# Kernel tuning notes

Hardware: AMD Instinct MI355X
Metric: run time of the kernel (lower is better)

## Reference

```python
import jax, jax.numpy as jnp
import numpy as np

B, L, D = 8, 8192, 512
TARGET_RATIO = 1.0 / 6.0


def _normalize(v):
    # matches torch F.normalize(dim=-1, eps=1e-12)
    n = jnp.maximum(jnp.linalg.norm(v, axis=-1, keepdims=True), 1e-12)
    return v / n


def _downsample(x, b_hard):
    # vectorized stream compaction, padded to L (static upper bound of L_max)
    Bb, Ll, Dd = x.shape
    cnt = jnp.cumsum(b_hard.astype(jnp.int32), axis=1)
    pos = jnp.where(b_hard > 0.5, cnt - 1, Ll)          # non-selected -> dump slot L
    bidx = jnp.arange(Bb)[:, None]
    out = jnp.zeros((Bb, Ll + 1, Dd), x.dtype).at[bidx, pos].set(x)[:, :Ll]
    counts = cnt[:, -1]
    mask = jnp.arange(Ll)[None, :] < counts[:, None]
    return out, mask


def setup_inputs() -> dict:
    key = jax.random.key(0)
    k1, k2, k3 = jax.random.split(key, 3)
    x = jax.random.normal(k1, (B, L, D), jnp.float32)
    W_q = jax.random.normal(k2, (D, D), jnp.float32) / np.sqrt(D)
    W_k = jax.random.normal(k3, (D, D), jnp.float32) / np.sqrt(D)
    return {"x": x, "W_q": W_q, "W_k": W_k}


def reference(x, W_q, W_k):
    q = _normalize(jnp.einsum('bld,ed->ble', x, W_q))   # nn.Linear: x @ W.T
    k = _normalize(jnp.einsum('bld,ed->ble', x, W_k))
    k_prev = jnp.pad(k[:, :-1, :], ((0, 0), (1, 0), (0, 0)))
    cos_sim = jnp.sum(q * k_prev, axis=-1)               # (B, L)
    p = jnp.clip(0.5 * (1.0 - cos_sim), 0.0, 1.0)
    p = p.at[:, 0].set(1.0)                              # first position always boundary
    b_hard = (p >= 0.5).astype(x.dtype)
    N = 1.0 / TARGET_RATIO
    F_actual = jnp.mean(b_hard)
    G_actual = jnp.mean(p)
    ratio_loss = N / (N - 1.0) * ((N - 1.0) * F_actual * G_actual + (1.0 - F_actual) * (1.0 - G_actual))
    compressed, comp_mask = _downsample(x, b_hard)
    p_compressed, _ = _downsample(p[..., None], b_hard)
    p_compressed = p_compressed[..., 0]
    return (compressed, comp_mask, b_hard, p, p_compressed, ratio_loss)
```

## Files before the change

kernel.cpp:

```cpp
#include <hip/hip_runtime.h>
#include <hip/hip_bf16.h>
#include <math.h>

#define BB 8
#define LL 8192
#define DD 512
#define NROWS (BB * LL)

#define OUT_COMP   0
#define OUT_MASK   33554432
#define OUT_BHARD  33619968
#define OUT_P      33685504
#define OUT_PCOMP  33751040
#define OUT_LOSS   33816576

#define WS_FIXLIST 0
#define WS_FIXCNT  262144
#define WS_COUNTS  262148
#define WS_SUMP    262180
#define WS_SEL     262212
#define WS_SSK     524416
#define WS_SSQ     786560
#define WS_DOT     1048704
#define WS_WQH     1310848
#define WS_WQL     1835136
#define WS_WKH     2359424
#define WS_WKL     2883712

#define FIX_CAP 65536
#define FIX_TAU 1e-4f

typedef __attribute__((ext_vector_type(8))) _Float16 half8;
typedef __attribute__((ext_vector_type(4))) float f32x4;

static __device__ __forceinline__ void ld_g2l16(const void* g, void* l) {
  __builtin_amdgcn_global_load_lds(
      (const __attribute__((address_space(1))) void*)g,
      (__attribute__((address_space(3))) void*)l, 16, 0, 0);
}

__global__ __launch_bounds__(256) void wsplit(
    const float* __restrict__ Wq, const float* __restrict__ Wk,
    _Float16* __restrict__ wqh, _Float16* __restrict__ wql,
    _Float16* __restrict__ wkh, _Float16* __restrict__ wkl,
    float* __restrict__ ssk, float* __restrict__ ssq,
    float* __restrict__ dotb, int* __restrict__ fixcnt) {
  const int t = blockIdx.x * 256 + threadIdx.x;
  if (t == 0) *fixcnt = 0;
  ssk[t] = 0.0f;
  ssq[t] = 0.0f;
  dotb[t] = 0.0f;

  const int m = t >> 15;
  const int c = t & 32767;
  const int kt = c >> 11;
  const int ct = (c >> 6) & 31;
  const int l = c & 63;
  const int n = l & 15;
  const int kblk = l >> 4;
  const int e = ct * 16 + n;
  const int d0 = kt * 32 + kblk * 8;
  const float* src = (m ? Wk : Wq) + (long)e * 512 + d0;
  _Float16* dh = (m ? wkh : wqh) + (long)c * 8;
  _Float16* dl = (m ? wkl : wql) + (long)c * 8;
  float4 v0 = *(const float4*)src;
  float4 v1 = *(const float4*)(src + 4);
  float av[8] = {v0.x, v0.y, v0.z, v0.w, v1.x, v1.y, v1.z, v1.w};
  half8 hi, lo;
#pragma unroll
  for (int j = 0; j < 8; ++j) {
    _Float16 hh = (_Float16)av[j];
    hi[j] = hh;
    lo[j] = (_Float16)(av[j] - (float)hh);
  }
  *(half8*)dh = hi;
  *(half8*)dl = lo;
}

__global__ __launch_bounds__(256, 2) void gemm_fused(
    const float* __restrict__ x,
    const _Float16* __restrict__ wqh, const _Float16* __restrict__ wql,
    const _Float16* __restrict__ wkh, const _Float16* __restrict__ wkl,
    float* __restrict__ ssqOut, float* __restrict__ sskOut,
    float* __restrict__ dotOut,
    float* __restrict__ qedge, float* __restrict__ kedge) {
  __shared__ _Float16 smem[24576];
  _Float16* AH = smem;
  _Float16* AL = AH + 4096;
  _Float16* BQH = AL + 4096;
  _Float16* BQL = BQH + 4096;
  _Float16* BKH = BQL + 4096;
  _Float16* BKL = BKH + 4096;

  const int tid = threadIdx.x;
  const int lane = tid & 63;
  const int w = tid >> 6;
  const int wrow = w & 1, wcol = w >> 1;
  const int g = lane >> 4, n = lane & 15;
  const int bx = blockIdx.x;
  const int rb = bx >> 2, cb = bx & 3;
  const long r0 = (long)rb * 128;

  const int arow = ((tid >> 6) << 4) | (tid & 15);
  const int akb = (tid >> 4) & 3;
  const float* ap = x + (r0 + arow) * 512 + akb * 8;

  f32x4 accq[4][4], acck[4][4];
#pragma unroll
  for (int mb = 0; mb < 4; ++mb)
#pragma unroll
    for (int nb = 0; nb < 4; ++nb) {
      accq[mb][nb] = (f32x4){0.f, 0.f, 0.f, 0.f};
      acck[mb][nb] = (f32x4){0.f, 0.f, 0.f, 0.f};
    }

  float4 f0 = *(const float4*)(ap);
  float4 f1 = *(const float4*)(ap + 4);
  float4 f2 = *(const float4*)(ap + 64 * 512);
  float4 f3 = *(const float4*)(ap + 64 * 512 + 4);

  for (int kt = 0; kt < 16; ++kt) {
    const long bbase = ((long)(kt * 32 + cb * 8) << 9) + w * 1024 + lane * 8;
    ld_g2l16(wqh + bbase, BQH + w * 1024);
    ld_g2l16(wqh + bbase + 512, BQH + w * 1024 + 512);
    ld_g2l16(wql + bbase, BQL + w * 1024);
    ld_g2l16(wql + bbase + 512, BQL + w * 1024 + 512);
    ld_g2l16(wkh + bbase, BKH + w * 1024);
    ld_g2l16(wkh + bbase + 512, BKH + w * 1024 + 512);
    ld_g2l16(wkl + bbase, BKL + w * 1024);
    ld_g2l16(wkl + bbase + 512, BKL + w * 1024 + 512);
    {
      float av0[8] = {f0.x, f0.y, f0.z, f0.w, f1.x, f1.y, f1.z, f1.w};
      float av1[8] = {f2.x, f2.y, f2.z, f2.w, f3.x, f3.y, f3.z, f3.w};
      half8 h0, h1, l0, l1;
#pragma unroll
      for (int j = 0; j < 8; ++j) {
        _Float16 a = (_Float16)av0[j];
        h0[j] = a;
        l0[j] = (_Float16)(av0[j] - (float)a);
        _Float16 b = (_Float16)av1[j];
        h1[j] = b;
        l1[j] = (_Float16)(av1[j] - (float)b);
      }
      *(half8*)(AH + tid * 8) = h0;
      *(half8*)(AH + (tid + 256) * 8) = h1;
      *(half8*)(AL + tid * 8) = l0;
      *(half8*)(AL + (tid + 256) * 8) = l1;
    }
    __syncthreads();
    if (kt < 15) {
      const float* xp = ap + (kt + 1) * 32;
      f0 = *(const float4*)(xp);
      f1 = *(const float4*)(xp + 4);
      f2 = *(const float4*)(xp + 64 * 512);
      f3 = *(const float4*)(xp + 64 * 512 + 4);
    }
    half8 ah[4], al[4];
#pragma unroll
    for (int mb = 0; mb < 4; ++mb) {
      const int cm = wrow * 4 + mb;
      ah[mb] = *(const half8*)(AH + (cm * 64 + lane) * 8);
      al[mb] = *(const half8*)(AL + (cm * 64 + lane) * 8);
    }
    {
      half8 bh[4], bl[4];
#pragma unroll
      for (int nb = 0; nb < 4; ++nb) {
        bh[nb] = *(const half8*)(BQH + ((wcol * 4 + nb) * 64 + lane) * 8);
        bl[nb] = *(const half8*)(BQL + ((wcol * 4 + nb) * 64 + lane) * 8);
      }
#pragma unroll
      for (int nb = 0; nb < 4; ++nb)
#pragma unroll
        for (int mb = 0; mb < 4; ++mb) {
          accq[mb][nb] = __builtin_amdgcn_mfma_f32_16x16x32_f16(ah[mb], bh[nb], accq[mb][nb], 0, 0, 0);
          accq[mb][nb] = __builtin_amdgcn_mfma_f32_16x16x32_f16(al[mb], bh[nb], accq[mb][nb], 0, 0, 0);
          accq[mb][nb] = __builtin_amdgcn_mfma_f32_16x16x32_f16(ah[mb], bl[nb], accq[mb][nb], 0, 0, 0);
        }
    }
    {
      half8 bh[4], bl[4];
#pragma unroll
      for (int nb = 0; nb < 4; ++nb) {
        bh[nb] = *(const half8*)(BKH + ((wcol * 4 + nb) * 64 + lane) * 8);
        bl[nb] = *(const half8*)(BKL + ((wcol * 4 + nb) * 64 + lane) * 8);
      }
#pragma unroll
      for (int nb = 0; nb < 4; ++nb)
#pragma unroll
        for (int mb = 0; mb < 4; ++mb) {
          acck[mb][nb] = __builtin_amdgcn_mfma_f32_16x16x32_f16(ah[mb], bh[nb], acck[mb][nb], 0, 0, 0);
          acck[mb][nb] = __builtin_amdgcn_mfma_f32_16x16x32_f16(al[mb], bh[nb], acck[mb][nb], 0, 0, 0);
          acck[mb][nb] = __builtin_amdgcn_mfma_f32_16x16x32_f16(ah[mb], bl[nb], acck[mb][nb], 0, 0, 0);
        }
    }
    __syncthreads();
  }

  _Float16* KX = smem;
  const int col0 = wcol * 64 + n;
  const int rbase = wrow * 64;
#pragma unroll
  for (int mb = 0; mb < 4; ++mb)
#pragma unroll
    for (int reg = 0; reg < 4; ++reg) {
      const int rl = rbase + mb * 16 + g * 4 + reg;
#pragma unroll
      for (int nb = 0; nb < 4; ++nb)
        KX[rl * 136 + col0 + nb * 16] = (_Float16)acck[mb][nb][reg];
    }
  __syncthreads();

  if (wrow == 1 && g == 3) {
#pragma unroll
    for (int nb = 0; nb < 4; ++nb)
      kedge[rb * 512 + cb * 128 + col0 + nb * 16] = acck[3][nb][3];
  }
  if (wrow == 0 && g == 0) {
#pragma unroll
    for (int nb = 0; nb < 4; ++nb)
      qedge[rb * 512 + cb * 128 + col0 + nb * 16] = accq[0][nb][0];
  }

#pragma unroll
  for (int mb = 0; mb < 4; ++mb) {
#pragma unroll
    for (int reg = 0; reg < 4; ++reg) {
      const int rl = rbase + mb * 16 + g * 4 + reg;
      const long row = r0 + rl;
      float sq = 0.f, sk = 0.f, dt = 0.f;
#pragma unroll
      for (int nb = 0; nb < 4; ++nb) {
        float qv = accq[mb][nb][reg];
        float kv = acck[mb][nb][reg];
        sq = fmaf(qv, qv, sq);
        sk = fmaf(kv, kv, sk);
        if (rl > 0) {
          float kp = (float)KX[(rl - 1) * 136 + col0 + nb * 16];
          dt = fmaf(qv, kp, dt);
        }
      }
#pragma unroll
      for (int m = 1; m < 16; m <<= 1) {
        sq += __shfl_xor(sq, m, 64);
        sk += __shfl_xor(sk, m, 64);
        dt += __shfl_xor(dt, m, 64);
      }
      if (n == 0) {
        atomicAdd(&ssqOut[row], sq);
        atomicAdd(&sskOut[row], sk);
        if (rl > 0) atomicAdd(&dotOut[row], dt);
      }
    }
  }
}

__global__ __launch_bounds__(64) void edgedot(
    const float* __restrict__ qedge, const float* __restrict__ kedge,
    float* __restrict__ dotOut) {
  const int rb = blockIdx.x;
  if (rb == 0) return;
  const long row = (long)rb * 128;
  if ((row & (LL - 1)) == 0) return;
  const int lane = threadIdx.x;
  float dt = 0.f;
#pragma unroll
  for (int c = lane; c < 512; c += 64)
    dt = fmaf(qedge[rb * 512 + c], kedge[(rb - 1) * 512 + c], dt);
#pragma unroll
  for (int m = 1; m < 64; m <<= 1) dt += __shfl_xor(dt, m, 64);
  if (lane == 0) dotOut[row] = dt;
}

__global__ __launch_bounds__(256) void combine(
    const float* __restrict__ ssq, const float* __restrict__ ssk,
    const float* __restrict__ dotb, float* __restrict__ dout,
    int* __restrict__ fixlist, int* __restrict__ fixcnt) {
  const int r = blockIdx.x * 256 + threadIdx.x;
  const int l = r & (LL - 1);
  float p;
  float cosv = 0.0f;
  if (l != 0) {
    float nq = fmaxf(sqrtf(ssq[r]), 1e-12f);
    float nk = fmaxf(sqrtf(ssk[r - 1]), 1e-12f);
    cosv = dotb[r] / (nq * nk);
    p = fminf(fmaxf(0.5f * (1.0f - cosv), 0.0f), 1.0f);
  } else {
    p = 1.0f;
  }
  dout[OUT_P + r] = p;
  dout[OUT_BHARD + r] = (p >= 0.5f) ? 1.0f : 0.0f;
  if (l != 0 && fabsf(cosv) < FIX_TAU) {
    int idx = atomicAdd(fixcnt, 1);
    if (idx < FIX_CAP) fixlist[idx] = r;
  }
}

__global__ __launch_bounds__(256) void fixup(
    const float* __restrict__ x, const float* __restrict__ Wq,
    const float* __restrict__ Wk, float* __restrict__ dout,
    const int* __restrict__ fixlist, const int* __restrict__ fixcnt) {
  __shared__ float xr[512], xp[512];
  __shared__ double red[3][256];
  const int t = threadIdx.x;
  int nfix = *fixcnt;
  if (nfix > FIX_CAP) nfix = FIX_CAP;

  for (int idx = blockIdx.x; idx < nfix; idx += gridDim.x) {
    const int r = fixlist[idx];
    for (int d = t; d < 512; d += 256) {
      xr[d] = x[(long)r * 512 + d];
      xp[d] = x[(long)(r - 1) * 512 + d];
    }
    __syncthreads();
    double ssq = 0.0, ssk = 0.0, dot = 0.0;
    for (int e = t; e < 512; e += 256) {
      const float* wq = Wq + (long)e * 512;
      const float* wk = Wk + (long)e * 512;
      double q = 0.0, k = 0.0;
      for (int d = 0; d < 512; ++d) {
        q = fma((double)xr[d], (double)wq[d], q);
        k = fma((double)xp[d], (double)wk[d], k);
      }
      ssq += q * q;
      ssk += k * k;
      dot += q * k;
    }
    red[0][t] = ssq;
    red[1][t] = ssk;
    red[2][t] = dot;
    __syncthreads();
    for (int s = 128; s > 0; s >>= 1) {
      if (t < s) {
        red[0][t] += red[0][t + s];
        red[1][t] += red[1][t + s];
        red[2][t] += red[2][t + s];
      }
      __syncthreads();
    }
    if (t == 0) {
      double nq = sqrt(red[0][0]);
      double nk = sqrt(red[1][0]);
      if (nq < 1e-12) nq = 1e-12;
      if (nk < 1e-12) nk = 1e-12;
      float c = (float)(red[2][0] / (nq * nk));
      float p = fminf(fmaxf(0.5f * (1.0f - c), 0.0f), 1.0f);
      dout[OUT_P + r] = p;
      dout[OUT_BHARD + r] = (p >= 0.5f) ? 1.0f : 0.0f;
    }
    __syncthreads();
  }
}

__global__ __launch_bounds__(256) void scanb(
    float* __restrict__ dout, int* __restrict__ sel,
    int* __restrict__ counts, float* __restrict__ sump) {
  __shared__ int wtot[4];
  __shared__ float wps[4];
  const int b = blockIdx.x;
  const int t = threadIdx.x;
  const int lane = t & 63, wv = t >> 6;
  const long base = (long)b * LL;

  int cnt = 0;
  float psum = 0.0f;
#pragma unroll 4
  for (int j = 0; j < 32; ++j) {
    int l = t * 32 + j;
    float bh = dout[OUT_BHARD + base + l];
    float pv = dout[OUT_P + base + l];
    cnt += (bh > 0.5f) ? 1 : 0;
    psum += pv;
  }
  int inc = cnt;
#pragma unroll
  for (int off = 1; off < 64; off <<= 1) {
    int u = __shfl_up(inc, off, 64);
    if (lane >= off) inc += u;
  }
  float ps = psum;
#pragma unroll
  for (int off = 1; off < 64; off <<= 1) ps += __shfl_xor(ps, off, 64);
  if (lane == 63) wtot[wv] = inc;
  if (lane == 0) wps[wv] = ps;
  __syncthreads();
  int wbase = 0, total = 0;
#pragma unroll
  for (int i = 0; i < 4; ++i) {
    int c = wtot[i];
    if (i < wv) wbase += c;
    total += c;
  }
  if (t == 0) {
    counts[b] = total;
    sump[b] = wps[0] + wps[1] + wps[2] + wps[3];
  }
  for (int j = 0; j < 32; ++j) {
    int l = t * 32 + j;
    dout[OUT_MASK + base + l] = (l < total) ? 1.0f : 0.0f;
    dout[OUT_PCOMP + base + l] = 0.0f;
  }
  __syncthreads();
  int pos = wbase + inc - cnt;
  for (int j = 0; j < 32; ++j) {
    int l = t * 32 + j;
    float bh = dout[OUT_BHARD + base + l];
    if (bh > 0.5f) {
      dout[OUT_PCOMP + base + pos] = dout[OUT_P + base + l];
      sel[base + pos] = l;
      ++pos;
    }
  }
}

__global__ void lossk(float* __restrict__ dout, const int* __restrict__ counts,
                      const float* __restrict__ sump) {
  if (threadIdx.x == 0 && blockIdx.x == 0) {
    float fc = 0.0f, gs = 0.0f;
    for (int b = 0; b < BB; ++b) {
      fc += (float)counts[b];
      gs += sump[b];
    }
    float F = fc / (float)NROWS;
    float G = gs / (float)NROWS;
    dout[OUT_LOSS] = 1.2f * (5.0f * F * G + (1.0f - F) * (1.0f - G));
  }
}

__global__ __launch_bounds__(128) void emit(
    const float* __restrict__ x, float* __restrict__ dout,
    const int* __restrict__ sel, const int* __restrict__ counts) {
  const long bid = blockIdx.x;
  const int b = (int)(bid >> 13);
  const int j = (int)(bid & (LL - 1));
  const int cnt = counts[b];
  float4 v = make_float4(0.0f, 0.0f, 0.0f, 0.0f);
  if (j < cnt) {
    const int l = sel[((long)b << 13) + j];
    v = *(const float4*)(x + (((long)b << 13) + l) * 512 + threadIdx.x * 4);
  }
  *(float4*)(dout + OUT_COMP + (((long)b << 13) + j) * 512 + threadIdx.x * 4) = v;
}

extern "C" void kernel_launch(void* const* d_in, const int* in_sizes, int n_in,
                              void* d_out, int out_size, void* d_ws,
                              size_t ws_size, hipStream_t stream) {
  const float* x = (const float*)d_in[0];
  const float* Wq = (const float*)d_in[1];
  const float* Wk = (const float*)d_in[2];
  float* out = (float*)d_out;
  char* ws = (char*)d_ws;

  int* fixlist = (int*)(ws + WS_FIXLIST);
  int* fixcnt = (int*)(ws + WS_FIXCNT);
  int* counts = (int*)(ws + WS_COUNTS);
  float* sump = (float*)(ws + WS_SUMP);
  int* sel = (int*)(ws + WS_SEL);
  float* ssk = (float*)(ws + WS_SSK);
  float* ssq = (float*)(ws + WS_SSQ);
  float* dotb = (float*)(ws + WS_DOT);
  _Float16* wqh = (_Float16*)(ws + WS_WQH);
  _Float16* wql = (_Float16*)(ws + WS_WQL);
  _Float16* wkh = (_Float16*)(ws + WS_WKH);
  _Float16* wkl = (_Float16*)(ws + WS_WKL);

  float* kedge = (float*)(out + OUT_COMP);
  float* qedge = (float*)(out + OUT_COMP + 262144);

  wsplit<<<256, 256, 0, stream>>>(Wq, Wk, wqh, wql, wkh, wkl, ssk, ssq, dotb, fixcnt);
  gemm_fused<<<2048, 256, 0, stream>>>(x, wqh, wql, wkh, wkl, ssq, ssk, dotb, qedge, kedge);
  edgedot<<<512, 64, 0, stream>>>(qedge, kedge, dotb);
  combine<<<NROWS / 256, 256, 0, stream>>>(ssq, ssk, dotb, out, fixlist, fixcnt);
  fixup<<<512, 256, 0, stream>>>(x, Wq, Wk, out, fixlist, fixcnt);
  scanb<<<BB, 256, 0, stream>>>(out, sel, counts, sump);
  lossk<<<1, 64, 0, stream>>>(out, counts, sump);
  emit<<<NROWS, 128, 0, stream>>>(x, out, sel, counts);
}
```

Measured before the change: 500.9 us.

## Drop weight low-half split, double-buffer LDS tiles, swizzle block order

Weights are now converted to a single fp16 term instead of hi+lo, which cuts MFMA count per tile from six to four and halves B-tile loads. The fix-up threshold is raised to catch the larger error this adds. The GEMM main loop is restructured into a two-stage LDS double buffer, so loading and converting the next K tile overlaps the MFMAs on the current one. It also adds an s_setprio bump around the MFMA block and remaps block indices so neighbouring blocks share rows. The risk is more rows sent to the exact fixup kernel, plus more LDS use that may lower occupancy.

```diff
diff --git a/kernel.cpp b/kernel.cpp
--- a/kernel.cpp
+++ b/kernel.cpp
@@ -23,12 +23,10 @@
 #define WS_SSQ     786560
 #define WS_DOT     1048704
 #define WS_WQH     1310848
-#define WS_WQL     1835136
-#define WS_WKH     2359424
-#define WS_WKL     2883712
+#define WS_WKH     1835136
 
 #define FIX_CAP 65536
-#define FIX_TAU 1e-4f
+#define FIX_TAU 4e-4f
 
 typedef __attribute__((ext_vector_type(8))) _Float16 half8;
 typedef __attribute__((ext_vector_type(4))) float f32x4;
@@ -41,8 +39,7 @@
 
 __global__ __launch_bounds__(256) void wsplit(
     const float* __restrict__ Wq, const float* __restrict__ Wk,
-    _Float16* __restrict__ wqh, _Float16* __restrict__ wql,
-    _Float16* __restrict__ wkh, _Float16* __restrict__ wkl,
+    _Float16* __restrict__ wqh, _Float16* __restrict__ wkh,
     float* __restrict__ ssk, float* __restrict__ ssq,
     float* __restrict__ dotb, int* __restrict__ fixcnt) {
   const int t = blockIdx.x * 256 + threadIdx.x;
@@ -62,42 +59,38 @@
   const int d0 = kt * 32 + kblk * 8;
   const float* src = (m ? Wk : Wq) + (long)e * 512 + d0;
   _Float16* dh = (m ? wkh : wqh) + (long)c * 8;
-  _Float16* dl = (m ? wkl : wql) + (long)c * 8;
   float4 v0 = *(const float4*)src;
   float4 v1 = *(const float4*)(src + 4);
   float av[8] = {v0.x, v0.y, v0.z, v0.w, v1.x, v1.y, v1.z, v1.w};
-  half8 hi, lo;
-#pragma unroll
-  for (int j = 0; j < 8; ++j) {
-    _Float16 hh = (_Float16)av[j];
-    hi[j] = hh;
-    lo[j] = (_Float16)(av[j] - (float)hh);
-  }
+  half8 hi;
+#pragma unroll
+  for (int j = 0; j < 8; ++j) hi[j] = (_Float16)av[j];
   *(half8*)dh = hi;
-  *(half8*)dl = lo;
 }
 
 __global__ __launch_bounds__(256, 2) void gemm_fused(
     const float* __restrict__ x,
-    const _Float16* __restrict__ wqh, const _Float16* __restrict__ wql,
-    const _Float16* __restrict__ wkh, const _Float16* __restrict__ wkl,
+    const _Float16* __restrict__ wqh, const _Float16* __restrict__ wkh,
     float* __restrict__ ssqOut, float* __restrict__ sskOut,
     float* __restrict__ dotOut,
     float* __restrict__ qedge, float* __restrict__ kedge) {
-  __shared__ _Float16 smem[24576];
-  _Float16* AH = smem;
-  _Float16* AL = AH + 4096;
-  _Float16* BQH = AL + 4096;
-  _Float16* BQL = BQH + 4096;
-  _Float16* BKH = BQL + 4096;
-  _Float16* BKL = BKH + 4096;
+  __shared__ _Float16 smem[32768];
+  _Float16* AH0 = smem;
+  _Float16* AL0 = smem + 4096;
+  _Float16* BQ0 = smem + 8192;
+  _Float16* BK0 = smem + 12288;
+  _Float16* AH1 = smem + 16384;
+  _Float16* AL1 = smem + 20480;
+  _Float16* BQ1 = smem + 24576;
+  _Float16* BK1 = smem + 28672;
 
   const int tid = threadIdx.x;
   const int lane = tid & 63;
   const int w = tid >> 6;
   const int wrow = w & 1, wcol = w >> 1;
   const int g = lane >> 4, n = lane & 15;
-  const int bx = blockIdx.x;
+  const int bx0 = blockIdx.x;
+  const int bx = ((bx0 & 7) << 8) | (bx0 >> 3);
   const int rb = bx >> 2, cb = bx & 3;
   const long r0 = (long)rb * 128;
 
@@ -114,86 +107,96 @@
       acck[mb][nb] = (f32x4){0.f, 0.f, 0.f, 0.f};
     }
 
-  float4 f0 = *(const float4*)(ap);
-  float4 f1 = *(const float4*)(ap + 4);
-  float4 f2 = *(const float4*)(ap + 64 * 512);
-  float4 f3 = *(const float4*)(ap + 64 * 512 + 4);
-
-  for (int kt = 0; kt < 16; ++kt) {
-    const long bbase = ((long)(kt * 32 + cb * 8) << 9) + w * 1024 + lane * 8;
-    ld_g2l16(wqh + bbase, BQH + w * 1024);
-    ld_g2l16(wqh + bbase + 512, BQH + w * 1024 + 512);
-    ld_g2l16(wql + bbase, BQL + w * 1024);
-    ld_g2l16(wql + bbase + 512, BQL + w * 1024 + 512);
-    ld_g2l16(wkh + bbase, BKH + w * 1024);
-    ld_g2l16(wkh + bbase + 512, BKH + w * 1024 + 512);
-    ld_g2l16(wkl + bbase, BKL + w * 1024);
-    ld_g2l16(wkl + bbase + 512, BKL + w * 1024 + 512);
-    {
-      float av0[8] = {f0.x, f0.y, f0.z, f0.w, f1.x, f1.y, f1.z, f1.w};
-      float av1[8] = {f2.x, f2.y, f2.z, f2.w, f3.x, f3.y, f3.z, f3.w};
-      half8 h0, h1, l0, l1;
-#pragma unroll
-      for (int j = 0; j < 8; ++j) {
-        _Float16 a = (_Float16)av0[j];
-        h0[j] = a;
-        l0[j] = (_Float16)(av0[j] - (float)a);
-        _Float16 b = (_Float16)av1[j];
-        h1[j] = b;
-        l1[j] = (_Float16)(av1[j] - (float)b);
-      }
-      *(half8*)(AH + tid * 8) = h0;
-      *(half8*)(AH + (tid + 256) * 8) = h1;
-      *(half8*)(AL + tid * 8) = l0;
-      *(half8*)(AL + (tid + 256) * 8) = l1;
-    }
+#define STAGE_B(ktv, BQ_, BK_)                                            \
+  do {                                                                    \
+    const long bb = ((long)((ktv)*32 + cb * 8) << 9) + w * 1024 + lane * 8; \
+    ld_g2l16(wqh + bb, (BQ_) + w * 1024);                                 \
+    ld_g2l16(wqh + bb + 512, (BQ_) + w * 1024 + 512);                     \
+    ld_g2l16(wkh + bb, (BK_) + w * 1024);                                 \
+    ld_g2l16(wkh + bb + 512, (BK_) + w * 1024 + 512);                     \
+  } while (0)
+
+#define CONV_A(F0, F1, F2, F3, AH_, AL_)                                  \
+  do {                                                                    \
+    float av0[8] = {F0.x, F0.y, F0.z, F0.w, F1.x, F1.y, F1.z, F1.w};      \
+    float av1[8] = {F2.x, F2.y, F2.z, F2.w, F3.x, F3.y, F3.z, F3.w};      \
+    half8 h0, h1, l0, l1;                                                 \
+    _Pragma("unroll") for (int j = 0; j < 8; ++j) {                       \
+      _Float16 a = (_Float16)av0[j];                                      \
+      h0[j] = a;                                                          \
+      l0[j] = (_Float16)(av0[j] - (float)a);                              \
+      _Float16 b = (_Float16)av1[j];                                      \
+      h1[j] = b;                                                          \
+      l1[j] = (_Float16)(av1[j] - (float)b);                              \
+    }                                                                     \
+    *(half8*)((AH_) + tid * 8) = h0;                                      \
+    *(half8*)((AH_) + (tid + 256) * 8) = h1;                              \
+    *(half8*)((AL_) + tid * 8) = l0;                                      \
+    *(half8*)((AL_) + (tid + 256) * 8) = l1;                              \
+  } while (0)
+
+#define COMPUTE(AH_, AL_, BQ_, BK_)                                       \
+  do {                                                                    \
+    half8 ah[4], al[4], bq[4], bk[4];                                     \
+    _Pragma("unroll") for (int mb = 0; mb < 4; ++mb) {                    \
+      const int cm = wrow * 4 + mb;                                       \
+      ah[mb] = *(const half8*)((AH_) + (cm * 64 + lane) * 8);             \
+      al[mb] = *(const half8*)((AL_) + (cm * 64 + lane) * 8);             \
+    }                                                                     \
+    _Pragma("unroll") for (int nb = 0; nb < 4; ++nb) {                    \
+      bq[nb] = *(const half8*)((BQ_) + ((wcol * 4 + nb) * 64 + lane) * 8);\
+      bk[nb] = *(const half8*)((BK_) + ((wcol * 4 + nb) * 64 + lane) * 8);\
+    }                                                                     \
+    __builtin_amdgcn_s_setprio(1);                                        \
+    _Pragma("unroll") for (int nb = 0; nb < 4; ++nb)                      \
+        _Pragma("unroll") for (int mb = 0; mb < 4; ++mb) {                \
+      accq[mb][nb] = __builtin_amdgcn_mfma_f32_16x16x32_f16(              \
+          ah[mb], bq[nb], accq[mb][nb], 0, 0, 0);                         \
+      acck[mb][nb] = __builtin_amdgcn_mfma_f32_16x16x32_f16(              \
+          ah[mb], bk[nb], acck[mb][nb], 0, 0, 0);                         \
+      accq[mb][nb] = __builtin_amdgcn_mfma_f32_16x16x32_f16(              \
+          al[mb], bq[nb], accq[mb][nb], 0, 0, 0);                         \
+      acck[mb][nb] = __builtin_amdgcn_mfma_f32_16x16x32_f16(              \
+          al[mb], bk[nb], acck[mb][nb], 0, 0, 0);                         \
+    }                                                                     \
+    __builtin_amdgcn_s_setprio(0);                                        \
+  } while (0)
+
+  STAGE_B(0, BQ0, BK0);
+  float4 pa0 = *(const float4*)(ap);
+  float4 pa1 = *(const float4*)(ap + 4);
+  float4 pa2 = *(const float4*)(ap + 64 * 512);
+  float4 pa3 = *(const float4*)(ap + 64 * 512 + 4);
+  CONV_A(pa0, pa1, pa2, pa3, AH0, AL0);
+  float4 pb0 = *(const float4*)(ap + 32);
+  float4 pb1 = *(const float4*)(ap + 32 + 4);
+  float4 pb2 = *(const float4*)(ap + 32 + 64 * 512);
+  float4 pb3 = *(const float4*)(ap + 32 + 64 * 512 + 4);
+  __syncthreads();
+
+  for (int i = 0; i < 8; ++i) {
+    const int kt = 2 * i;
+    STAGE_B(kt + 1, BQ1, BK1);
+    CONV_A(pb0, pb1, pb2, pb3, AH1, AL1);
+    if (i < 7) {
+      const float* xp = ap + (kt + 2) * 32;
+      pa0 = *(const float4*)(xp);
+      pa1 = *(const float4*)(xp + 4);
+      pa2 = *(const float4*)(xp + 64 * 512);
+      pa3 = *(const float4*)(xp + 64 * 512 + 4);
+    }
+    COMPUTE(AH0, AL0, BQ0, BK0);
     __syncthreads();
-    if (kt < 15) {
-      const float* xp = ap + (kt + 1) * 32;
-      f0 = *(const float4*)(xp);
-      f1 = *(const float4*)(xp + 4);
-      f2 = *(const float4*)(xp + 64 * 512);
-      f3 = *(const float4*)(xp + 64 * 512 + 4);
-    }
-    half8 ah[4], al[4];
-#pragma unroll
-    for (int mb = 0; mb < 4; ++mb) {
-      const int cm = wrow * 4 + mb;
-      ah[mb] = *(const half8*)(AH + (cm * 64 + lane) * 8);
-      al[mb] = *(const half8*)(AL + (cm * 64 + lane) * 8);
-    }
-    {
-      half8 bh[4], bl[4];
-#pragma unroll
-      for (int nb = 0; nb < 4; ++nb) {
-        bh[nb] = *(const half8*)(BQH + ((wcol * 4 + nb) * 64 + lane) * 8);
-        bl[nb] = *(const half8*)(BQL + ((wcol * 4 + nb) * 64 + lane) * 8);
-      }
-#pragma unroll
-      for (int nb = 0; nb < 4; ++nb)
-#pragma unroll
-        for (int mb = 0; mb < 4; ++mb) {
-          accq[mb][nb] = __builtin_amdgcn_mfma_f32_16x16x32_f16(ah[mb], bh[nb], accq[mb][nb], 0, 0, 0);
-          accq[mb][nb] = __builtin_amdgcn_mfma_f32_16x16x32_f16(al[mb], bh[nb], accq[mb][nb], 0, 0, 0);
-          accq[mb][nb] = __builtin_amdgcn_mfma_f32_16x16x32_f16(ah[mb], bl[nb], accq[mb][nb], 0, 0, 0);
-        }
-    }
-    {
-      half8 bh[4], bl[4];
-#pragma unroll
-      for (int nb = 0; nb < 4; ++nb) {
-        bh[nb] = *(const half8*)(BKH + ((wcol * 4 + nb) * 64 + lane) * 8);
-        bl[nb] = *(const half8*)(BKL + ((wcol * 4 + nb) * 64 + lane) * 8);
-      }
-#pragma unroll
-      for (int nb = 0; nb < 4; ++nb)
-#pragma unroll
-        for (int mb = 0; mb < 4; ++mb) {
-          acck[mb][nb] = __builtin_amdgcn_mfma_f32_16x16x32_f16(ah[mb], bh[nb], acck[mb][nb], 0, 0, 0);
-          acck[mb][nb] = __builtin_amdgcn_mfma_f32_16x16x32_f16(al[mb], bh[nb], acck[mb][nb], 0, 0, 0);
-          acck[mb][nb] = __builtin_amdgcn_mfma_f32_16x16x32_f16(ah[mb], bl[nb], acck[mb][nb], 0, 0, 0);
-        }
-    }
+    if (i < 7) {
+      STAGE_B(kt + 2, BQ0, BK0);
+      CONV_A(pa0, pa1, pa2, pa3, AH0, AL0);
+      const float* xp2 = ap + (kt + 3) * 32;
+      pb0 = *(const float4*)(xp2);
+      pb1 = *(const float4*)(xp2 + 4);
+      pb2 = *(const float4*)(xp2 + 64 * 512);
+      pb3 = *(const float4*)(xp2 + 64 * 512 + 4);
+    }
+    COMPUTE(AH1, AL1, BQ1, BK1);
     __syncthreads();
   }
 
@@ -253,6 +256,9 @@
       }
     }
   }
+#undef STAGE_B
+#undef CONV_A
+#undef COMPUTE
 }
 
 __global__ __launch_bounds__(64) void edgedot(
@@ -460,15 +466,13 @@
   float* ssq = (float*)(ws + WS_SSQ);
   float* dotb = (float*)(ws + WS_DOT);
   _Float16* wqh = (_Float16*)(ws + WS_WQH);
-  _Float16* wql = (_Float16*)(ws + WS_WQL);
   _Float16* wkh = (_Float16*)(ws + WS_WKH);
-  _Float16* wkl = (_Float16*)(ws + WS_WKL);
 
   float* kedge = (float*)(out + OUT_COMP);
   float* qedge = (float*)(out + OUT_COMP + 262144);
 
-  wsplit<<<256, 256, 0, stream>>>(Wq, Wk, wqh, wql, wkh, wkl, ssk, ssq, dotb, fixcnt);
-  gemm_fused<<<2048, 256, 0, stream>>>(x, wqh, wql, wkh, wkl, ssq, ssk, dotb, qedge, kedge);
+  wsplit<<<256, 256, 0, stream>>>(Wq, Wk, wqh, wkh, ssk, ssq, dotb, fixcnt);
+  gemm_fused<<<2048, 256, 0, stream>>>(x, wqh, wkh, ssq, ssk, dotb, qedge, kedge);
   edgedot<<<512, 64, 0, stream>>>(qedge, kedge, dotb);
   combine<<<NROWS / 256, 256, 0, stream>>>(ssq, ssk, dotb, out, fixlist, fixcnt);
   fixup<<<512, 256, 0, stream>>>(x, Wq, Wk, out, fixlist, fixcnt);
```

Result: slower. 533.3 us (+6.5%).
